# Kernel tuning notes

Hardware: AMD Instinct MI355X
Metric: run time of the kernel (lower is better)

## Reference

```python
import jax, jax.numpy as jnp
import numpy as np

BATCH = 1024
D_MODEL = 1024
HEADS = 16
D_K = D_MODEL // HEADS  # 64


def setup_inputs() -> dict:
    key = jax.random.key(0)
    ks = jax.random.split(key, 8)
    s = 1.0 / np.sqrt(D_MODEL)
    return {
        "x": jax.random.normal(ks[0], (BATCH, D_MODEL), dtype=jnp.float32),
        "weights": jax.random.normal(ks[1], (BATCH, HEADS, D_K, D_K), dtype=jnp.float32),
        "Wq": jax.random.normal(ks[2], (D_MODEL, HEADS * D_K), dtype=jnp.float32) * s,
        "Wk": jax.random.normal(ks[3], (D_MODEL, HEADS * D_K), dtype=jnp.float32) * s,
        "Wv": jax.random.normal(ks[4], (D_MODEL, HEADS * D_K), dtype=jnp.float32) * s,
        "Wg": jax.random.normal(ks[5], (D_MODEL, HEADS), dtype=jnp.float32) * s,
        "Wo": jax.random.normal(ks[6], (D_MODEL, D_MODEL), dtype=jnp.float32) * s,
        "bo": jnp.zeros((D_MODEL,), dtype=jnp.float32),
    }


def reference(x, weights, Wq, Wk, Wv, Wg, Wo, bo):
    b = x.shape[0]
    h, dv, dk = weights.shape[1], weights.shape[2], weights.shape[3]
    # projections -> [b, h, d_k]; sigma is identity in this module
    q = (x @ Wq).reshape(b, h, dk)
    k = (x @ Wk).reshape(b, h, dk)
    v = (x @ Wv).reshape(b, h, dv)
    # gate beta: [b, h, 1]
    beta = jax.nn.sigmoid(x @ Wg)[:, :, None]
    # read existing value from fast-weight memory
    v_existing = jnp.einsum('bhvk,bhk->bhv', weights, k)
    # outer-product delta-rule write
    new_weights = weights + jnp.einsum('bhv,bhk->bhvk', beta * (v - v_existing), k)
    # read with query
    out = jnp.einsum('bhvk,bhk->bhv', new_weights, q).reshape(b, h * dv)
    out = out @ Wo + bo
    return (out, new_weights)
```

## Files before the change

kernel.cpp:

```cpp
#include <hip/hip_runtime.h>

#define BATCH 1024
#define DMODEL 1024
#define HEADS 16

typedef short bh8 __attribute__((ext_vector_type(8)));
typedef float f4 __attribute__((ext_vector_type(4)));
typedef unsigned short u16x4 __attribute__((ext_vector_type(4)));

__device__ inline unsigned short f2b(float f) {
  union { float f; unsigned int u; } x; x.f = f;
  unsigned int r = x.u + 0x7fffu + ((x.u >> 16) & 1u);
  return (unsigned short)(r >> 16);
}

__global__ __launch_bounds__(256)
void prep_kernel(const float* __restrict__ x,
                 const float* __restrict__ Wq, const float* __restrict__ Wk,
                 const float* __restrict__ Wv, const float* __restrict__ Wo,
                 const float* __restrict__ Wg,
                 unsigned short* __restrict__ xh, unsigned short* __restrict__ WqkvT,
                 unsigned short* __restrict__ WoT, float* __restrict__ betab) {
  __shared__ float sm[32 * 33];
  const int blk = blockIdx.x;
  if (blk < 4096) {
    const int mat = blk >> 10, id = blk & 1023;
    const float* src = (mat == 0) ? Wq : (mat == 1) ? Wk : (mat == 2) ? Wv : Wo;
    unsigned short* dst = (mat < 3) ? (WqkvT + (size_t)mat * 1024 * 1024) : WoT;
    const int c0 = (id & 31) * 32, r0 = (id >> 5) * 32;
    const int tx = threadIdx.x & 31, ty = threadIdx.x >> 5;
    #pragma unroll
    for (int i = ty; i < 32; i += 8)
      sm[i * 33 + tx] = src[(size_t)(r0 + i) * 1024 + c0 + tx];
    __syncthreads();
    #pragma unroll
    for (int i = ty; i < 32; i += 8)
      dst[(size_t)(c0 + i) * 1024 + r0 + tx] = f2b(sm[tx * 33 + i]);
  } else if (blk < 5120) {
    const int i = (blk - 4096) * 256 + threadIdx.x;
    const float4 f = ((const float4*)x)[i];
    u16x4 hv = { f2b(f.x), f2b(f.y), f2b(f.z), f2b(f.w) };
    ((u16x4*)xh)[i] = hv;
  } else {
    const int b = blk - 5120;
    float* xr = sm;
    for (int i = threadIdx.x; i < DMODEL; i += 256) xr[i] = x[(size_t)b * DMODEL + i];
    __syncthreads();
    const int wid = threadIdx.x >> 6, lane = threadIdx.x & 63;
    #pragma unroll
    for (int hh = 0; hh < 4; ++hh) {
      const int h = wid * 4 + hh;
      float p = 0.f;
      for (int i = lane; i < DMODEL; i += 64) p += xr[i] * Wg[(size_t)i * HEADS + h];
      #pragma unroll
      for (int off = 32; off > 0; off >>= 1) p += __shfl_down(p, off, 64);
      if (lane == 0) betab[b * HEADS + h] = 1.f / (1.f + __expf(-p));
    }
  }
}

template<int BM, int BN>
__global__ __launch_bounds__(256)
void gemm_tn(const unsigned short* __restrict__ A, const unsigned short* __restrict__ Bt,
             float* __restrict__ C, const float* __restrict__ bias, int N, int K) {
  constexpr int BK = 32;
  constexpr int LD = BK + 8;
  constexpr int TM = BM / 32;
  constexpr int TN = BN / 32;
  __shared__ unsigned short As[BM * LD];
  __shared__ unsigned short Bs[BN * LD];
  const int tid = threadIdx.x;
  const int lane = tid & 63;
  const int wid = tid >> 6;
  const int wm = wid >> 1, wn = wid & 1;
  const int m0 = blockIdx.y * BM, n0 = blockIdx.x * BN;
  const int row16 = lane & 15;
  const int quad = lane >> 4;
  const int s_chunk = tid & 3, s_row = tid >> 2;

  f4 acc[TM][TN];
  #pragma unroll
  for (int i = 0; i < TM; ++i)
    #pragma unroll
    for (int j = 0; j < TN; ++j)
      acc[i][j] = f4{0.f, 0.f, 0.f, 0.f};

  for (int k0 = 0; k0 < K; k0 += BK) {
    #pragma unroll
    for (int p = 0; p < BM / 64; ++p) {
      int r = s_row + p * 64;
      bh8 v = *(const bh8*)(A + (size_t)(m0 + r) * K + k0 + s_chunk * 8);
      *(bh8*)(&As[r * LD + s_chunk * 8]) = v;
    }
    #pragma unroll
    for (int p = 0; p < BN / 64; ++p) {
      int r = s_row + p * 64;
      bh8 v = *(const bh8*)(Bt + (size_t)(n0 + r) * K + k0 + s_chunk * 8);
      *(bh8*)(&Bs[r * LD + s_chunk * 8]) = v;
    }
    __syncthreads();
    bh8 af[TM], bfr[TN];
    #pragma unroll
    for (int i = 0; i < TM; ++i)
      af[i] = *(const bh8*)(&As[(wm * (BM / 2) + i * 16 + row16) * LD + quad * 8]);
    #pragma unroll
    for (int j = 0; j < TN; ++j)
      bfr[j] = *(const bh8*)(&Bs[(wn * (BN / 2) + j * 16 + row16) * LD + quad * 8]);
    #pragma unroll
    for (int i = 0; i < TM; ++i)
      #pragma unroll
      for (int j = 0; j < TN; ++j)
        acc[i][j] = __builtin_amdgcn_mfma_f32_16x16x32_bf16(af[i], bfr[j], acc[i][j], 0, 0, 0);
    __syncthreads();
  }
  #pragma unroll
  for (int i = 0; i < TM; ++i) {
    #pragma unroll
    for (int j = 0; j < TN; ++j) {
      int col = n0 + wn * (BN / 2) + j * 16 + row16;
      float bv = bias ? bias[col] : 0.f;
      #pragma unroll
      for (int rg = 0; rg < 4; ++rg) {
        int row = m0 + wm * (BM / 2) + i * 16 + quad * 4 + rg;
        C[(size_t)row * N + col] = acc[i][j][rg] + bv;
      }
    }
  }
}

__global__ __launch_bounds__(256)
void fastweight_kernel(const float* __restrict__ Wf, const float* __restrict__ QKV,
                       const float* __restrict__ beta, float* __restrict__ newW,
                       unsigned short* __restrict__ hiddenh) {
  const int bh = blockIdx.x;
  const int b = bh >> 4, h = bh & 15;
  const int t = threadIdx.x;
  const int seg = t & 15;
  const int rbase = t >> 4;
  const float* base = QKV + (size_t)b * 3072 + h * 64;
  const float4 qq = ((const float4*)base)[seg];
  const float4 kk = ((const float4*)(base + 1024))[seg];
  const float be = beta[bh];
  const float4* wp = (const float4*)(Wf + (size_t)bh * 4096);
  float4* op = (float4*)(newW + (size_t)bh * 4096);

  float4 w[4];
  #pragma unroll
  for (int j = 0; j < 4; ++j) w[j] = wp[t + 256 * j];

  float vex[4];
  #pragma unroll
  for (int j = 0; j < 4; ++j) {
    float p = w[j].x * kk.x + w[j].y * kk.y + w[j].z * kk.z + w[j].w * kk.w;
    p += __shfl_xor(p, 1, 64);
    p += __shfl_xor(p, 2, 64);
    p += __shfl_xor(p, 4, 64);
    p += __shfl_xor(p, 8, 64);
    vex[j] = p;
  }
  #pragma unroll
  for (int j = 0; j < 4; ++j) {
    const int r = rbase + 16 * j;
    const float dv = be * (base[2048 + r] - vex[j]);
    w[j].x += dv * kk.x; w[j].y += dv * kk.y;
    w[j].z += dv * kk.z; w[j].w += dv * kk.w;
    op[t + 256 * j] = w[j];
    float o = w[j].x * qq.x + w[j].y * qq.y + w[j].z * qq.z + w[j].w * qq.w;
    o += __shfl_xor(o, 1, 64);
    o += __shfl_xor(o, 2, 64);
    o += __shfl_xor(o, 4, 64);
    o += __shfl_xor(o, 8, 64);
    if (seg == 0) hiddenh[(size_t)b * DMODEL + h * 64 + r] = f2b(o);
  }
}

extern "C" void kernel_launch(void* const* d_in, const int* in_sizes, int n_in,
                              void* d_out, int out_size, void* d_ws, size_t ws_size,
                              hipStream_t stream) {
  const float* x  = (const float*)d_in[0];
  const float* Wf = (const float*)d_in[1];
  const float* Wq = (const float*)d_in[2];
  const float* Wk = (const float*)d_in[3];
  const float* Wv = (const float*)d_in[4];
  const float* Wg = (const float*)d_in[5];
  const float* Wo = (const float*)d_in[6];
  const float* bo = (const float*)d_in[7];
  float* out  = (float*)d_out;
  float* newW = out + (size_t)BATCH * DMODEL;

  unsigned short* xh      = (unsigned short*)d_ws;
  unsigned short* WqkvT   = xh + (size_t)1024 * 1024;
  unsigned short* WoT     = WqkvT + (size_t)3072 * 1024;
  unsigned short* hiddenh = WoT + (size_t)1024 * 1024;
  float* QKV   = (float*)(hiddenh + (size_t)1024 * 1024);
  float* betab = QKV + (size_t)1024 * 3072;

  prep_kernel<<<6144, 256, 0, stream>>>(x, Wq, Wk, Wv, Wo, Wg, xh, WqkvT, WoT, betab);
  gemm_tn<64, 64><<<dim3(3072 / 64, 1024 / 64), 256, 0, stream>>>(xh, WqkvT, QKV, nullptr, 3072, 1024);
  fastweight_kernel<<<BATCH * HEADS, 256, 0, stream>>>(Wf, QKV, betab, newW, hiddenh);
  gemm_tn<64, 64><<<dim3(1024 / 64, 1024 / 64), 256, 0, stream>>>(hiddenh, WoT, out, bo, 1024, 1024);
}
```

Baseline: 559.9 us.

## Load GEMM tiles via global_load_lds and enlarge QKV GEMM tiles

```diff
diff --git a/kernel.cpp b/kernel.cpp
--- a/kernel.cpp
+++ b/kernel.cpp
@@ -7,6 +7,9 @@
 typedef short bh8 __attribute__((ext_vector_type(8)));
 typedef float f4 __attribute__((ext_vector_type(4)));
 typedef unsigned short u16x4 __attribute__((ext_vector_type(4)));
+
+typedef __attribute__((address_space(1))) const void gvoid;
+typedef __attribute__((address_space(3))) void lvoid;
 
 __device__ inline unsigned short f2b(float f) {
   union { float f; unsigned int u; } x; x.f = f;
@@ -61,14 +64,15 @@
 
 template<int BM, int BN>
 __global__ __launch_bounds__(256)
-void gemm_tn(const unsigned short* __restrict__ A, const unsigned short* __restrict__ Bt,
-             float* __restrict__ C, const float* __restrict__ bias, int N, int K) {
+void gemm_lds(const unsigned short* __restrict__ A, const unsigned short* __restrict__ Bt,
+              float* __restrict__ C, const float* __restrict__ bias, int N, int K) {
   constexpr int BK = 32;
-  constexpr int LD = BK + 8;
   constexpr int TM = BM / 32;
   constexpr int TN = BN / 32;
-  __shared__ unsigned short As[BM * LD];
-  __shared__ unsigned short Bs[BN * LD];
+  constexpr int PA = (BM * 64) / 4096;
+  constexpr int PB = (BN * 64) / 4096;
+  __shared__ unsigned short As[BM * BK];
+  __shared__ unsigned short Bs[BN * BK];
   const int tid = threadIdx.x;
   const int lane = tid & 63;
   const int wid = tid >> 6;
@@ -76,7 +80,6 @@
   const int m0 = blockIdx.y * BM, n0 = blockIdx.x * BN;
   const int row16 = lane & 15;
   const int quad = lane >> 4;
-  const int s_chunk = tid & 3, s_row = tid >> 2;
 
   f4 acc[TM][TN];
   #pragma unroll
@@ -87,25 +90,29 @@
 
   for (int k0 = 0; k0 < K; k0 += BK) {
     #pragma unroll
-    for (int p = 0; p < BM / 64; ++p) {
-      int r = s_row + p * 64;
-      bh8 v = *(const bh8*)(A + (size_t)(m0 + r) * K + k0 + s_chunk * 8);
-      *(bh8*)(&As[r * LD + s_chunk * 8]) = v;
-    }
-    #pragma unroll
-    for (int p = 0; p < BN / 64; ++p) {
-      int r = s_row + p * 64;
-      bh8 v = *(const bh8*)(Bt + (size_t)(n0 + r) * K + k0 + s_chunk * 8);
-      *(bh8*)(&Bs[r * LD + s_chunk * 8]) = v;
+    for (int p = 0; p < PA; ++p) {
+      const int o = p * 4096 + tid * 16;
+      const int r = o >> 6, ch = (o & 63) >> 1;
+      __builtin_amdgcn_global_load_lds(
+          (gvoid*)(A + (size_t)(m0 + r) * K + k0 + ch),
+          (lvoid*)((char*)As + o), 16, 0, 0);
+    }
+    #pragma unroll
+    for (int p = 0; p < PB; ++p) {
+      const int o = p * 4096 + tid * 16;
+      const int r = o >> 6, ch = (o & 63) >> 1;
+      __builtin_amdgcn_global_load_lds(
+          (gvoid*)(Bt + (size_t)(n0 + r) * K + k0 + ch),
+          (lvoid*)((char*)Bs + o), 16, 0, 0);
     }
     __syncthreads();
     bh8 af[TM], bfr[TN];
     #pragma unroll
     for (int i = 0; i < TM; ++i)
-      af[i] = *(const bh8*)(&As[(wm * (BM / 2) + i * 16 + row16) * LD + quad * 8]);
+      af[i] = *(const bh8*)(&As[(wm * (BM / 2) + i * 16 + row16) * BK + quad * 8]);
     #pragma unroll
     for (int j = 0; j < TN; ++j)
-      bfr[j] = *(const bh8*)(&Bs[(wn * (BN / 2) + j * 16 + row16) * LD + quad * 8]);
+      bfr[j] = *(const bh8*)(&Bs[(wn * (BN / 2) + j * 16 + row16) * BK + quad * 8]);
     #pragma unroll
     for (int i = 0; i < TM; ++i)
       #pragma unroll
@@ -196,7 +203,7 @@
   float* betab = QKV + (size_t)1024 * 3072;
 
   prep_kernel<<<6144, 256, 0, stream>>>(x, Wq, Wk, Wv, Wo, Wg, xh, WqkvT, WoT, betab);
-  gemm_tn<64, 64><<<dim3(3072 / 64, 1024 / 64), 256, 0, stream>>>(xh, WqkvT, QKV, nullptr, 3072, 1024);
+  gemm_lds<128, 128><<<dim3(3072 / 128, 1024 / 128), 256, 0, stream>>>(xh, WqkvT, QKV, nullptr, 3072, 1024);
   fastweight_kernel<<<BATCH * HEADS, 256, 0, stream>>>(Wf, QKV, betab, newW, hiddenh);
-  gemm_tn<64, 64><<<dim3(1024 / 64, 1024 / 64), 256, 0, stream>>>(hiddenh, WoT, out, bo, 1024, 1024);
-}
+  gemm_lds<64, 64><<<dim3(1024 / 64, 1024 / 64), 256, 0, stream>>>(hiddenh, WoT, out, bo, 1024, 1024);
+}
```

Result: no change. 561.1 us (+0.2%).
